# Kernel optimization log

Hardware: AMD Instinct MI355X
Metric: run time of the kernel (lower is better)

## Reference

```python
import jax, jax.numpy as jnp
import numpy as np
from jax.scipy.special import gammaln

N_NODES = 50000
N_EDGES = 1600000
IN_DIM, H1, H2 = 512, 256, 129  # H2 = hid_dims[-1] + 1 (kappa column)


def setup_inputs() -> dict:
    key = jax.random.key(0)
    k1, k2, k3, k4 = jax.random.split(key, 4)
    x = jax.random.normal(k1, (N_NODES, IN_DIM), dtype=jnp.float32)
    edge_index = jax.random.randint(k2, (2, N_EDGES), 0, N_NODES, dtype=jnp.int32)
    # Glorot-ish init for GCN weights
    W0 = jax.random.normal(k3, (IN_DIM, H1), dtype=jnp.float32) * (1.0 / np.sqrt(IN_DIM))
    W1 = jax.random.normal(k4, (H1, H2), dtype=jnp.float32) * (1.0 / np.sqrt(H1))
    return {"x": x, "edge_index": edge_index, "W0": W0, "W1": W1}


def _gcn_conv(h, W, src, dst, norm, n):
    # PyG GCNConv (bias=False): h' = D^-1/2 (A+I) D^-1/2 (h W)
    h = h @ W
    msg = h[src] * norm[:, None]          # [E+N, F_out]
    return jax.ops.segment_sum(msg, dst, num_segments=n)


def reference(x, edge_index, W0, W1):
    n = x.shape[0]
    loops = jnp.arange(n, dtype=edge_index.dtype)
    src = jnp.concatenate([edge_index[0], loops])
    dst = jnp.concatenate([edge_index[1], loops])
    # symmetric normalization with self-loops (deg >= 1, so rsqrt is safe)
    deg = jax.ops.segment_sum(jnp.ones_like(dst, dtype=x.dtype), dst, num_segments=n)
    dinv = jax.lax.rsqrt(deg)
    norm = dinv[src] * dinv[dst]          # [E+N]

    h = jax.nn.softplus(_gcn_conv(x, W0, src, dst, norm, n))
    # dropout is identity in eval mode (training=False)
    h = jax.nn.softplus(_gcn_conv(h, W1, src, dst, norm, n))

    lbd = h[:, :-1]                       # [N, 128] Weibull scale
    kappa = h[:, -1:] + 0.1               # [N, 1]   Weibull shape
    # deterministic (non-random-encoder / eval) reparameterization:
    # z = lbd * exp(lgamma(1 + 1/kappa))  == E[Weibull(lbd, kappa)]
    z = lbd * jnp.exp(gammaln(1.0 + 1.0 / kappa))
    return z, lbd, kappa
```

## Files before the change

### kernel.cpp

```cpp
#include <hip/hip_runtime.h>
#include <hip/hip_bf16.h>
#include <math.h>


typedef unsigned short ushort_t;
typedef __attribute__((ext_vector_type(8))) short bf16x8;
typedef __attribute__((ext_vector_type(4))) float f32x4;

#define BSH 9
#define MAXB 128

__device__ __forceinline__ ushort_t f2bf(float f) {
    union { float f; unsigned u; } x; x.f = f;
    unsigned r = x.u + 0x7FFF + ((x.u >> 16) & 1);
    return (ushort_t)(r >> 16);
}
__device__ __forceinline__ float bf2f(ushort_t s) {
    union { unsigned u; float f; } x; x.u = ((unsigned)s) << 16; return x.f;
}

__device__ __forceinline__ void async_copy16(const void* gsrc, void* ldst) {
    __builtin_amdgcn_global_load_lds(
        (const __attribute__((address_space(1))) unsigned int*)gsrc,
        (__attribute__((address_space(3))) unsigned int*)ldst,
        16, 0, 0);
}


__global__ __launch_bounds__(256) void bucket_count(const int* __restrict__ dst,
                                                    int* __restrict__ btot,
                                                    int E, int nbk)
{
    __shared__ int hist[MAXB];
    int tid = threadIdx.x;
    int per = (E + gridDim.x - 1) / gridDim.x;
    int lo  = blockIdx.x * per;
    int hi  = min(lo + per, E);
    for (int i = tid; i < nbk; i += 256) hist[i] = 0;
    __syncthreads();
    for (int i = lo + tid; i < hi; i += 256)
        atomicAdd(&hist[dst[i] >> BSH], 1);
    __syncthreads();
    for (int i = tid; i < nbk; i += 256)
        if (hist[i]) atomicAdd(&btot[i], hist[i]);
}

__global__ __launch_bounds__(128) void scan98(const int* __restrict__ btot,
                                              int* __restrict__ bstart,
                                              int* __restrict__ bcursor, int nbk)
{
    __shared__ int ws[2];
    int tid = threadIdx.x, lane = tid & 63, wid = tid >> 6;
    int v = (tid < nbk) ? btot[tid] : 0;
    int s = v;
#pragma unroll
    for (int off = 1; off < 64; off <<= 1) {
        int t = __shfl_up(s, off, 64);
        if (lane >= off) s += t;
    }
    if (lane == 63) ws[wid] = s;
    __syncthreads();
    int excl = s - v + ((wid == 1) ? ws[0] : 0);
    if (tid < nbk) { bstart[tid] = excl; bcursor[tid] = excl; }
    if (tid == nbk - 1) bstart[nbk] = excl + v;
}

__global__ __launch_bounds__(256) void partition_kernel(const int* __restrict__ src,
                                                        const int* __restrict__ dst,
                                                        int* __restrict__ bcursor,
                                                        int* __restrict__ stage,
                                                        int E, int nbk)
{
    __shared__ int hist[MAXB];
    int tid = threadIdx.x;
    int per = (E + gridDim.x - 1) / gridDim.x;
    int lo  = blockIdx.x * per;
    int hi  = min(lo + per, E);
    for (int i = tid; i < nbk; i += 256) hist[i] = 0;
    __syncthreads();
    for (int i = lo + tid; i < hi; i += 256)
        atomicAdd(&hist[dst[i] >> BSH], 1);
    __syncthreads();
    for (int i = tid; i < nbk; i += 256) {
        int c = hist[i];
        hist[i] = c ? atomicAdd(&bcursor[i], c) : 0;
    }
    __syncthreads();
    for (int i = lo + tid; i < hi; i += 256) {
        int d = dst[i], s = src[i];
        int pos = atomicAdd(&hist[d >> BSH], 1);
        stage[pos] = ((d & ((1 << BSH) - 1)) << 16) | s;
    }
}

__global__ __launch_bounds__(256) void buildcsr(const int* __restrict__ stage,
                                                const int* __restrict__ bstart,
                                                int* __restrict__ rowptr,
                                                float* __restrict__ dinv,
                                                int* __restrict__ col,
                                                int N, int E)
{
    __shared__ int hist[512];
    __shared__ int excl[512];
    __shared__ int wsum[4];
    int g = blockIdx.x, tid = threadIdx.x;
    int ebeg = bstart[g], eend = bstart[g + 1];

    for (int i = tid; i < 512; i += 256) hist[i] = 0;
    __syncthreads();
    for (int i = ebeg + tid; i < eend; i += 256)
        atomicAdd(&hist[stage[i] >> 16], 1);
    __syncthreads();

    int h0 = hist[2 * tid], h1 = hist[2 * tid + 1];
    int ps = h0 + h1;
    int lane = tid & 63, wid = tid >> 6;
    int s = ps;
#pragma unroll
    for (int off = 1; off < 64; off <<= 1) {
        int t = __shfl_up(s, off, 64);
        if (lane >= off) s += t;
    }
    if (lane == 63) wsum[wid] = s;
    __syncthreads();
    if (tid < 4) {
        int w = wsum[tid];
#pragma unroll
        for (int off = 1; off < 4; off <<= 1) {
            int t = __shfl_up(w, off, 64);
            if (tid >= off) w += t;
        }
        wsum[tid] = w;
    }
    __syncthreads();
    int ex = s - ps + (wid ? wsum[wid - 1] : 0);
    excl[2 * tid]     = ex;
    excl[2 * tid + 1] = ex + h0;

    int nb0 = g << BSH;
#pragma unroll
    for (int q = 0; q < 2; ++q) {
        int binv = 2 * tid + q;
        int node = nb0 + binv;
        if (node < N) {
            rowptr[node] = ebeg + ((q == 0) ? ex : ex + h0);
            dinv[node]   = rsqrtf((float)(((q == 0) ? h0 : h1) + 1));
        }
    }
    if (g == gridDim.x - 1 && tid == 0) rowptr[N] = E;

    __syncthreads();
    for (int i = tid; i < 512; i += 256) hist[i] = ebeg + excl[i];
    __syncthreads();
    for (int i = ebeg + tid; i < eend; i += 256) {
        int p = stage[i];
        int pos = atomicAdd(&hist[p >> 16], 1);
        col[pos] = p & 0xFFFF;
    }
}


__global__ __launch_bounds__(256) void conv_x(const float* __restrict__ x,
                                              ushort_t* __restrict__ Abig,
                                              int M, int M_pad)
{
    int id = blockIdx.x * blockDim.x + threadIdx.x;
    int r = id >> 7, q = id & 127;
    if (r >= M_pad) return;
    float4 v = make_float4(0.f, 0.f, 0.f, 0.f);
    if (r < M) v = *reinterpret_cast<const float4*>(&x[(size_t)r * 512 + q * 4]);
    ushort4 h, l;
    h.x = f2bf(v.x); l.x = f2bf(v.x - bf2f(h.x));
    h.y = f2bf(v.y); l.y = f2bf(v.y - bf2f(h.y));
    h.z = f2bf(v.z); l.z = f2bf(v.z - bf2f(h.z));
    h.w = f2bf(v.w); l.w = f2bf(v.w - bf2f(h.w));
    ushort_t* rowp = Abig + (size_t)r * 1024;
    *reinterpret_cast<ushort4*>(rowp + q * 4)       = h;
    *reinterpret_cast<ushort4*>(rowp + 512 + q * 4) = l;
}

__global__ __launch_bounds__(256) void conv_w0(const float* __restrict__ W0,
                                               ushort_t* __restrict__ BT)
{
    int id = blockIdx.x * blockDim.x + threadIdx.x;
    int k = id & 511, n = id >> 9;
    if (n >= 256) return;
    float v = W0[(size_t)k * 256 + n];
    ushort_t h = f2bf(v);
    ushort_t l = f2bf(v - bf2f(h));
    ushort_t* rowp = BT + (size_t)n * 1536;
    rowp[k] = h; rowp[512 + k] = h; rowp[1024 + k] = l;
}

__global__ __launch_bounds__(256) void conv_w1(const float* __restrict__ W1,
                                               ushort_t* __restrict__ BT,
                                               float* __restrict__ W1col)
{
    int id = blockIdx.x * blockDim.x + threadIdx.x;
    int k = id & 255, n = id >> 8;
    if (n >= 128) return;
    float v = W1[(size_t)k * 129 + n];
    ushort_t h = f2bf(v);
    ushort_t l = f2bf(v - bf2f(h));
    ushort_t* rowp = BT + (size_t)n * 768;
    rowp[k] = h; rowp[256 + k] = h; rowp[512 + k] = l;
    if (n == 0) W1col[k] = W1[(size_t)k * 129 + 128];
}

__global__ __launch_bounds__(256) void gemm_bf16(const ushort_t* __restrict__ A, int lda,
                                                 const ushort_t* __restrict__ BT, int ldbt,
                                                 float* __restrict__ C, int ldc,
                                                 int M, int K, int kwrap,
                                                 const float* __restrict__ rowscale)
{
    __shared__ short As[128 * 32];
    __shared__ short Bs[128 * 32];

    int tid  = threadIdx.x;
    int w    = tid >> 6;
    int lane = tid & 63;
    int lm   = lane & 15;
    int lq   = lane >> 4;
    int bm   = blockIdx.x * 128;
    int bn   = blockIdx.y * 128;
    int wr   = (w >> 1) * 64;
    int wc   = (w & 1) * 64;

    f32x4 acc[4][4];
#pragma unroll
    for (int i = 0; i < 4; ++i)
#pragma unroll
        for (int j = 0; j < 4; ++j) acc[i][j] = (f32x4)(0.f);

    int srow = (lane >> 2);
    int scol = (lane & 3) * 16;

    for (int k0 = 0; k0 < K; k0 += 32) {
        int ka = (k0 < kwrap) ? k0 : (k0 - kwrap);
#pragma unroll
        for (int q = 0; q < 2; ++q) {
            int r = w * 32 + q * 16 + srow;
            const char* ga = (const char*)A + ((size_t)(bm + r) * lda + ka) * 2 + scol;
            async_copy16(ga, (char*)As + (size_t)(w * 32 + q * 16) * 64);
        }
#pragma unroll
        for (int q = 0; q < 2; ++q) {
            int r = w * 32 + q * 16 + srow;
            const char* gb = (const char*)BT + ((size_t)(bn + r) * ldbt + k0) * 2 + scol;
            async_copy16(gb, (char*)Bs + (size_t)(w * 32 + q * 16) * 64);
        }
        __syncthreads();

        bf16x8 afr[4], bfr[4];
#pragma unroll
        for (int mi = 0; mi < 4; ++mi)
            afr[mi] = *reinterpret_cast<const bf16x8*>(&As[(wr + mi * 16 + lm) * 32 + lq * 8]);
#pragma unroll
        for (int ni = 0; ni < 4; ++ni)
            bfr[ni] = *reinterpret_cast<const bf16x8*>(&Bs[(wc + ni * 16 + lm) * 32 + lq * 8]);
#pragma unroll
        for (int mi = 0; mi < 4; ++mi)
#pragma unroll
            for (int ni = 0; ni < 4; ++ni)
                acc[mi][ni] = __builtin_amdgcn_mfma_f32_16x16x32_bf16(
                    afr[mi], bfr[ni], acc[mi][ni], 0, 0, 0);
        __syncthreads();
    }

#pragma unroll
    for (int mi = 0; mi < 4; ++mi) {
        int rbase = bm + wr + mi * 16 + lq * 4;
        float rs[4];
#pragma unroll
        for (int e = 0; e < 4; ++e)
            rs[e] = (rbase + e < M) ? rowscale[rbase + e] : 0.f;
#pragma unroll
        for (int ni = 0; ni < 4; ++ni) {
            int cc = bn + wc + ni * 16 + lm;
#pragma unroll
            for (int e = 0; e < 4; ++e) {
                int r = rbase + e;
                if (r < M) C[(size_t)r * ldc + cc] = acc[mi][ni][e] * rs[e];
            }
        }
    }
}


__device__ __forceinline__ float softplus_f(float x)
{
    return fmaxf(x, 0.f) + log1pf(expf(-fabsf(x)));
}

__device__ __forceinline__ void add4(float4& a, const float4& v)
{
    a.x += v.x; a.y += v.y; a.z += v.z; a.w += v.w;
}

__device__ __forceinline__ void add2(float2& a, const float2& v)
{
    a.x += v.x; a.y += v.y;
}

__global__ __launch_bounds__(256) void agg1_kernel(const float* __restrict__ T1s,
                                                   const float* __restrict__ dinv,
                                                   const int* __restrict__ rowptr,
                                                   const int* __restrict__ col,
                                                   const float* __restrict__ W1col,
                                                   ushort_t* __restrict__ H1big,
                                                   float* __restrict__ T2k,
                                                   int node0, int node1)
{
    int wslot = __builtin_amdgcn_readfirstlane(threadIdx.x >> 6);
    int node  = node0 + blockIdx.x * 4 + wslot;
    if (node >= node1) return;
    int lane = threadIdx.x & 63;
    float di = dinv[node];
    int beg = rowptr[node], end = rowptr[node + 1];

    float4 a0 = make_float4(0.f, 0.f, 0.f, 0.f);
    float4 a1 = a0, a2 = a0, a3 = a0;

    const float* Trow = T1s + (size_t)lane * 4;

    int e = beg;
    for (; e + 4 <= end; e += 4) {
        int s0 = col[e], s1 = col[e + 1], s2 = col[e + 2], s3 = col[e + 3];
        float4 v0 = *reinterpret_cast<const float4*>(Trow + (size_t)s0 * 256);
        float4 v1 = *reinterpret_cast<const float4*>(Trow + (size_t)s1 * 256);
        float4 v2 = *reinterpret_cast<const float4*>(Trow + (size_t)s2 * 256);
        float4 v3 = *reinterpret_cast<const float4*>(Trow + (size_t)s3 * 256);
        add4(a0, v0); add4(a1, v1); add4(a2, v2); add4(a3, v3);
    }
    for (; e < end; ++e) {
        int s = col[e];
        float4 v = *reinterpret_cast<const float4*>(Trow + (size_t)s * 256);
        add4(a0, v);
    }

    float4 self = *reinterpret_cast<const float4*>(Trow + (size_t)node * 256);
    float4 o;
    o.x = softplus_f((a0.x + a1.x + a2.x + a3.x + self.x) * di);
    o.y = softplus_f((a0.y + a1.y + a2.y + a3.y + self.y) * di);
    o.z = softplus_f((a0.z + a1.z + a2.z + a3.z + self.z) * di);
    o.w = softplus_f((a0.w + a1.w + a2.w + a3.w + self.w) * di);

    ushort4 h, l;
    h.x = f2bf(o.x); l.x = f2bf(o.x - bf2f(h.x));
    h.y = f2bf(o.y); l.y = f2bf(o.y - bf2f(h.y));
    h.z = f2bf(o.z); l.z = f2bf(o.z - bf2f(h.z));
    h.w = f2bf(o.w); l.w = f2bf(o.w - bf2f(h.w));
    ushort_t* rowp = H1big + (size_t)node * 512;
    *reinterpret_cast<ushort4*>(rowp + lane * 4)       = h;
    *reinterpret_cast<ushort4*>(rowp + 256 + lane * 4) = l;

    float4 wv = *reinterpret_cast<const float4*>(&W1col[lane * 4]);
    float tk = o.x * wv.x + o.y * wv.y + o.z * wv.z + o.w * wv.w;
#pragma unroll
    for (int off = 32; off > 0; off >>= 1)
        tk += __shfl_down(tk, off, 64);
    if (lane == 0) T2k[node] = tk * di;
}

__global__ __launch_bounds__(256) void agg2_kernel(const float* __restrict__ T2s,
                                                   const float* __restrict__ T2k,
                                                   const float* __restrict__ dinv,
                                                   const int* __restrict__ rowptr,
                                                   const int* __restrict__ col,
                                                   float* __restrict__ z_out,
                                                   float* __restrict__ lbd_out,
                                                   float* __restrict__ kap_out, int N)
{
    int wslot = __builtin_amdgcn_readfirstlane(threadIdx.x >> 6);
    int node  = blockIdx.x * 4 + wslot;
    if (node >= N) return;
    int lane = threadIdx.x & 63;
    float di = dinv[node];
    int beg = rowptr[node], end = rowptr[node + 1];

    float2 a0 = make_float2(0.f, 0.f);
    float2 a1 = a0, a2 = a0, a3 = a0;
    float k0 = 0.f, k1 = 0.f, k2 = 0.f, k3 = 0.f;

    const float* Trow = T2s + (size_t)lane * 2;

    int e = beg;
    for (; e + 4 <= end; e += 4) {
        int s0 = col[e], s1 = col[e + 1], s2 = col[e + 2], s3 = col[e + 3];
        k0 += T2k[s0]; k1 += T2k[s1]; k2 += T2k[s2]; k3 += T2k[s3];
        float2 v0 = *reinterpret_cast<const float2*>(Trow + (size_t)s0 * 128);
        float2 v1 = *reinterpret_cast<const float2*>(Trow + (size_t)s1 * 128);
        float2 v2 = *reinterpret_cast<const float2*>(Trow + (size_t)s2 * 128);
        float2 v3 = *reinterpret_cast<const float2*>(Trow + (size_t)s3 * 128);
        add2(a0, v0); add2(a1, v1); add2(a2, v2); add2(a3, v3);
    }
    for (; e < end; ++e) {
        int s = col[e];
        k0 += T2k[s];
        float2 v = *reinterpret_cast<const float2*>(Trow + (size_t)s * 128);
        add2(a0, v);
    }

    float2 self = *reinterpret_cast<const float2*>(Trow + (size_t)node * 128);
    float2 sp;
    sp.x = softplus_f((a0.x + a1.x + a2.x + a3.x + self.x) * di);
    sp.y = softplus_f((a0.y + a1.y + a2.y + a3.y + self.y) * di);

    float ak = ((k0 + k1 + k2 + k3) + T2k[node]) * di;
    float kv = softplus_f(ak) + 0.1f;
    float g  = expf(lgammaf(1.0f + 1.0f / kv));
    if (lane == 0) kap_out[node] = kv;

    size_t o = (size_t)node * 128 + lane * 2;
    float2 zv = make_float2(sp.x * g, sp.y * g);
    *reinterpret_cast<float2*>(&lbd_out[o]) = sp;
    *reinterpret_cast<float2*>(&z_out[o])   = zv;
}

extern "C" void kernel_launch(void* const* d_in, const int* in_sizes, int n_in,
                              void* d_out, int out_size, void* d_ws, size_t ws_size,
                              hipStream_t stream)
{
    const float* x  = (const float*)d_in[0];
    const int*   ei = (const int*)d_in[1];
    const float* W0 = (const float*)d_in[2];
    const float* W1 = (const float*)d_in[3];

    const int N = in_sizes[0] / 512;
    const int E = in_sizes[1] / 2;
    const int* src = ei;
    const int* dst = ei + E;

    const int mblocks = (N + 127) / 128;
    const int M_pad   = mblocks * 128;
    const int nbk     = (N + 511) >> BSH;

    char* w = (char*)d_ws;
    size_t off = 0;
    auto take = [&](size_t bytes) -> void* {
        void* p = (void*)(w + off);
        off = (off + bytes + 255) & ~(size_t)255;
        return p;
    };
    int*      rowptr = (int*)take((size_t)(N + 1) * 4);
    float*    dinv   = (float*)take((size_t)N * 4);
    int*      col    = (int*)take((size_t)E * 4);
    int*      stage  = (int*)take((size_t)E * 4);
    int*      btot   = (int*)take((size_t)MAXB * 4);
    int*      bstart = (int*)take((size_t)(MAXB + 1) * 4);
    int*      bcursor= (int*)take((size_t)MAXB * 4);
    ushort_t* W0bigT = (ushort_t*)take((size_t)256 * 1536 * 2);
    ushort_t* W1bigT = (ushort_t*)take((size_t)128 * 768 * 2);
    float*    W1col  = (float*)take((size_t)256 * 4);
    float*    T2k    = (float*)take((size_t)N * 4);
    float*    T1     = (float*)take((size_t)N * 256 * 4);
    float*    T2     = T1;
    ushort_t* Abig   = (ushort_t*)take((size_t)M_pad * 1024 * 2);
    ushort_t* H1big  = Abig;

    float* z_out   = (float*)d_out;
    float* lbd_out = z_out + (size_t)N * 128;
    float* kap_out = lbd_out + (size_t)N * 128;

    hipMemsetAsync(btot, 0, (size_t)MAXB * 4, stream);
    bucket_count<<<256, 256, 0, stream>>>(dst, btot, E, nbk);
    scan98<<<1, 128, 0, stream>>>(btot, bstart, bcursor, nbk);
    partition_kernel<<<256, 256, 0, stream>>>(src, dst, bcursor, stage, E, nbk);
    buildcsr<<<nbk, 256, 0, stream>>>(stage, bstart, rowptr, dinv, col, N, E);

    conv_x<<<(M_pad * 128) / 256, 256, 0, stream>>>(x, Abig, N, M_pad);
    conv_w0<<<(256 * 512) / 256, 256, 0, stream>>>(W0, W0bigT);
    conv_w1<<<(128 * 256) / 256, 256, 0, stream>>>(W1, W1bigT, W1col);

    dim3 g1(mblocks, 2);
    gemm_bf16<<<g1, 256, 0, stream>>>(Abig, 1024, W0bigT, 1536, T1, 256, N, 1536, 1024, dinv);

    const int half = ((N / 2) + 3) & ~3;
    agg1_kernel<<<(half + 3) / 4, 256, 0, stream>>>(T1, dinv, rowptr, col, W1col,
                                                    H1big, T2k, 0, half);
    agg1_kernel<<<(N - half + 3) / 4, 256, 0, stream>>>(T1, dinv, rowptr, col, W1col,
                                                        H1big, T2k, half, N);

    dim3 g2(mblocks, 1);
    gemm_bf16<<<g2, 256, 0, stream>>>(H1big, 512, W1bigT, 768, T2, 128, N, 768, 512, dinv);

    agg2_kernel<<<(N + 3) / 4, 256, 0, stream>>>(T2, T2k, dinv, rowptr, col,
                                                 z_out, lbd_out, kap_out, N);
}
```

Measured before the change: 730.5 us.

## Fuse x fp32-to-bf16 split conversion into first GEMM with full-N tile

Removes the separate conv_x pass that wrote a hi/lo bf16 copy of x, and instead converts x tiles to hi/lo bf16 in registers while loading them into LDS inside a new 512-thread GEMM that covers all 256 output columns per block. This avoids writing and re-reading the expanded bf16 A buffer and reads x only once instead of once per column block. The A path is now synchronous global loads plus conversion, with no async overlap. H1big gets its own buffer, and agg2 is split into two launches over node halves.

```diff
diff --git a/kernel.cpp b/kernel.cpp
--- a/kernel.cpp
+++ b/kernel.cpp
@@ -159,25 +159,6 @@
     }
 }
 
-
-__global__ __launch_bounds__(256) void conv_x(const float* __restrict__ x,
-                                              ushort_t* __restrict__ Abig,
-                                              int M, int M_pad)
-{
-    int id = blockIdx.x * blockDim.x + threadIdx.x;
-    int r = id >> 7, q = id & 127;
-    if (r >= M_pad) return;
-    float4 v = make_float4(0.f, 0.f, 0.f, 0.f);
-    if (r < M) v = *reinterpret_cast<const float4*>(&x[(size_t)r * 512 + q * 4]);
-    ushort4 h, l;
-    h.x = f2bf(v.x); l.x = f2bf(v.x - bf2f(h.x));
-    h.y = f2bf(v.y); l.y = f2bf(v.y - bf2f(h.y));
-    h.z = f2bf(v.z); l.z = f2bf(v.z - bf2f(h.z));
-    h.w = f2bf(v.w); l.w = f2bf(v.w - bf2f(h.w));
-    ushort_t* rowp = Abig + (size_t)r * 1024;
-    *reinterpret_cast<ushort4*>(rowp + q * 4)       = h;
-    *reinterpret_cast<ushort4*>(rowp + 512 + q * 4) = l;
-}
 
 __global__ __launch_bounds__(256) void conv_w0(const float* __restrict__ W0,
                                                ushort_t* __restrict__ BT)
@@ -207,6 +188,103 @@
     if (n == 0) W1col[k] = W1[(size_t)k * 129 + 128];
 }
 
+__global__ __launch_bounds__(512) void gemm1_fused(const float* __restrict__ x,
+                                                   const ushort_t* __restrict__ BT,
+                                                   float* __restrict__ C,
+                                                   int M,
+                                                   const float* __restrict__ rowscale)
+{
+    __shared__ short Ah[128 * 32];
+    __shared__ short Al[128 * 32];
+    __shared__ short Bh[256 * 32];
+    __shared__ short Bl[256 * 32];
+
+    int tid  = threadIdx.x;
+    int w    = tid >> 6;
+    int lane = tid & 63;
+    int lm   = lane & 15;
+    int lq   = lane >> 4;
+    int bm   = blockIdx.x * 128;
+    int wr   = (w >> 2) * 64;
+    int wc   = (w & 3) * 64;
+
+    f32x4 acc[4][4];
+#pragma unroll
+    for (int i = 0; i < 4; ++i)
+#pragma unroll
+        for (int j = 0; j < 4; ++j) acc[i][j] = (f32x4)(0.f);
+
+    int arow = tid >> 3;
+    int acol = (tid & 7) * 4;
+
+    for (int kc = 0; kc < 512; kc += 32) {
+#pragma unroll
+        for (int p = 0; p < 2; ++p) {
+            int r  = arow + p * 64;
+            int rg = bm + r;
+            float4 v = make_float4(0.f, 0.f, 0.f, 0.f);
+            if (rg < M) v = *reinterpret_cast<const float4*>(&x[(size_t)rg * 512 + kc + acol]);
+            ushort4 h, l;
+            h.x = f2bf(v.x); l.x = f2bf(v.x - bf2f(h.x));
+            h.y = f2bf(v.y); l.y = f2bf(v.y - bf2f(h.y));
+            h.z = f2bf(v.z); l.z = f2bf(v.z - bf2f(h.z));
+            h.w = f2bf(v.w); l.w = f2bf(v.w - bf2f(h.w));
+            *reinterpret_cast<ushort4*>(&Ah[r * 32 + acol]) = h;
+            *reinterpret_cast<ushort4*>(&Al[r * 32 + acol]) = l;
+        }
+#pragma unroll
+        for (int p = 0; p < 2; ++p) {
+            int row = w * 16 + p * 128 + (lane >> 2);
+            int seg = lane & 3;
+            const char* gh = (const char*)BT + ((size_t)row * 1536 + kc) * 2 + seg * 16;
+            async_copy16(gh, (char*)Bh + (size_t)row * 64 + seg * 16);
+            const char* gl = (const char*)BT + ((size_t)row * 1536 + 1024 + kc) * 2 + seg * 16;
+            async_copy16(gl, (char*)Bl + (size_t)row * 64 + seg * 16);
+        }
+        __syncthreads();
+
+        bf16x8 ah[4], al[4];
+#pragma unroll
+        for (int mi = 0; mi < 4; ++mi) {
+            ah[mi] = *reinterpret_cast<const bf16x8*>(&Ah[(wr + mi * 16 + lm) * 32 + lq * 8]);
+            al[mi] = *reinterpret_cast<const bf16x8*>(&Al[(wr + mi * 16 + lm) * 32 + lq * 8]);
+        }
+#pragma unroll
+        for (int ni = 0; ni < 4; ++ni) {
+            bf16x8 bh = *reinterpret_cast<const bf16x8*>(&Bh[(wc + ni * 16 + lm) * 32 + lq * 8]);
+            bf16x8 bl = *reinterpret_cast<const bf16x8*>(&Bl[(wc + ni * 16 + lm) * 32 + lq * 8]);
+#pragma unroll
+            for (int mi = 0; mi < 4; ++mi)
+                acc[mi][ni] = __builtin_amdgcn_mfma_f32_16x16x32_bf16(ah[mi], bh, acc[mi][ni], 0, 0, 0);
+#pragma unroll
+            for (int mi = 0; mi < 4; ++mi)
+                acc[mi][ni] = __builtin_amdgcn_mfma_f32_16x16x32_bf16(al[mi], bh, acc[mi][ni], 0, 0, 0);
+#pragma unroll
+            for (int mi = 0; mi < 4; ++mi)
+                acc[mi][ni] = __builtin_amdgcn_mfma_f32_16x16x32_bf16(ah[mi], bl, acc[mi][ni], 0, 0, 0);
+        }
+        __syncthreads();
+    }
+
+#pragma unroll
+    for (int mi = 0; mi < 4; ++mi) {
+        int rbase = bm + wr + mi * 16 + lq * 4;
+        float rs[4];
+#pragma unroll
+        for (int e = 0; e < 4; ++e)
+            rs[e] = (rbase + e < M) ? rowscale[rbase + e] : 0.f;
+#pragma unroll
+        for (int ni = 0; ni < 4; ++ni) {
+            int cc = wc + ni * 16 + lm;
+#pragma unroll
+            for (int e = 0; e < 4; ++e) {
+                int r = rbase + e;
+                if (r < M) C[(size_t)r * 256 + cc] = acc[mi][ni][e] * rs[e];
+            }
+        }
+    }
+}
+
 __global__ __launch_bounds__(256) void gemm_bf16(const ushort_t* __restrict__ A, int lda,
                                                  const ushort_t* __restrict__ BT, int ldbt,
                                                  float* __restrict__ C, int ldc,
@@ -369,11 +447,12 @@
                                                    const int* __restrict__ col,
                                                    float* __restrict__ z_out,
                                                    float* __restrict__ lbd_out,
-                                                   float* __restrict__ kap_out, int N)
+                                                   float* __restrict__ kap_out,
+                                                   int node0, int node1)
 {
     int wslot = __builtin_amdgcn_readfirstlane(threadIdx.x >> 6);
-    int node  = blockIdx.x * 4 + wslot;
-    if (node >= N) return;
+    int node  = node0 + blockIdx.x * 4 + wslot;
+    if (node >= node1) return;
     int lane = threadIdx.x & 63;
     float di = dinv[node];
     int beg = rowptr[node], end = rowptr[node + 1];
@@ -455,8 +534,7 @@
     float*    T2k    = (float*)take((size_t)N * 4);
     float*    T1     = (float*)take((size_t)N * 256 * 4);
     float*    T2     = T1;
-    ushort_t* Abig   = (ushort_t*)take((size_t)M_pad * 1024 * 2);
-    ushort_t* H1big  = Abig;
+    ushort_t* H1big  = (ushort_t*)take((size_t)M_pad * 512 * 2);
 
     float* z_out   = (float*)d_out;
     float* lbd_out = z_out + (size_t)N * 128;
@@ -468,12 +546,10 @@
     partition_kernel<<<256, 256, 0, stream>>>(src, dst, bcursor, stage, E, nbk);
     buildcsr<<<nbk, 256, 0, stream>>>(stage, bstart, rowptr, dinv, col, N, E);
 
-    conv_x<<<(M_pad * 128) / 256, 256, 0, stream>>>(x, Abig, N, M_pad);
     conv_w0<<<(256 * 512) / 256, 256, 0, stream>>>(W0, W0bigT);
     conv_w1<<<(128 * 256) / 256, 256, 0, stream>>>(W1, W1bigT, W1col);
 
-    dim3 g1(mblocks, 2);
-    gemm_bf16<<<g1, 256, 0, stream>>>(Abig, 1024, W0bigT, 1536, T1, 256, N, 1536, 1024, dinv);
+    gemm1_fused<<<mblocks, 512, 0, stream>>>(x, W0bigT, T1, N, dinv);
 
     const int half = ((N / 2) + 3) & ~3;
     agg1_kernel<<<(half + 3) / 4, 256, 0, stream>>>(T1, dinv, rowptr, col, W1col,
@@ -484,6 +560,8 @@
     dim3 g2(mblocks, 1);
     gemm_bf16<<<g2, 256, 0, stream>>>(H1big, 512, W1bigT, 768, T2, 128, N, 768, 512, dinv);
 
-    agg2_kernel<<<(N + 3) / 4, 256, 0, stream>>>(T2, T2k, dinv, rowptr, col,
-                                                 z_out, lbd_out, kap_out, N);
-}
+    agg2_kernel<<<(half + 3) / 4, 256, 0, stream>>>(T2, T2k, dinv, rowptr, col,
+                                                    z_out, lbd_out, kap_out, 0, half);
+    agg2_kernel<<<(N - half + 3) / 4, 256, 0, stream>>>(T2, T2k, dinv, rowptr, col,
+                                                        z_out, lbd_out, kap_out, half, N);
+}
```

After: 703.1 us. 3.8% less time.
